# Kernel optimization log

Hardware: AMD Instinct MI355X
Metric: run time of the kernel (lower is better)

Reference implementation:

```python
import jax, jax.numpy as jnp
import numpy as np

B, A, S, IN, H, OUT, T = 32768, 10, 50, 6, 64, 2, 60


def _p(key, shape, scale=0.1):
    return (jax.random.normal(key, shape) * scale).astype(jnp.float32)


def setup_inputs() -> dict:
    key = jax.random.key(0)
    ks = jax.random.split(key, 20)
    inp = {
        'history': jax.random.normal(ks[0], (B, A, S, IN), dtype=jnp.float32),
        # encoder layer 0 (IN->H) and layer 1 (H->H); PyTorch gate order i,f,g,o
        'enc_Wih0': _p(ks[1], (4 * H, IN)), 'enc_Whh0': _p(ks[2], (4 * H, H)),
        'enc_bih0': _p(ks[3], (4 * H,)),    'enc_bhh0': _p(ks[4], (4 * H,)),
        'enc_Wih1': _p(ks[5], (4 * H, H)),  'enc_Whh1': _p(ks[6], (4 * H, H)),
        'enc_bih1': _p(ks[7], (4 * H,)),    'enc_bhh1': _p(ks[8], (4 * H,)),
        # decoder layer 0 (OUT->H) and layer 1 (H->H)
        'dec_Wih0': _p(ks[9], (4 * H, OUT)), 'dec_Whh0': _p(ks[10], (4 * H, H)),
        'dec_bih0': _p(ks[11], (4 * H,)),    'dec_bhh0': _p(ks[12], (4 * H,)),
        'dec_Wih1': _p(ks[13], (4 * H, H)),  'dec_Whh1': _p(ks[14], (4 * H, H)),
        'dec_bih1': _p(ks[15], (4 * H,)),    'dec_bhh1': _p(ks[16], (4 * H,)),
        'lin_W': _p(ks[17], (OUT, H)), 'lin_b': _p(ks[18], (OUT,)),
        'start_token': _p(ks[19], (1, 1, OUT)),
    }
    return inp


def _cell(x, h, c, Wih, Whh, bih, bhh):
    g = x @ Wih.T + h @ Whh.T + (bih + bhh)
    i, f, gg, o = jnp.split(g, 4, axis=-1)
    c2 = jax.nn.sigmoid(f) * c + jax.nn.sigmoid(i) * jnp.tanh(gg)
    h2 = jax.nn.sigmoid(o) * jnp.tanh(c2)
    return h2, c2


def reference(history, enc_Wih0, enc_Whh0, enc_bih0, enc_bhh0,
              enc_Wih1, enc_Whh1, enc_bih1, enc_bhh1,
              dec_Wih0, dec_Whh0, dec_bih0, dec_bhh0,
              dec_Wih1, dec_Whh1, dec_bih1, dec_bhh1,
              lin_W, lin_b, start_token):
    ego = history[:, 0]                     # [B, S, IN]
    b = ego.shape[0]
    z = jnp.zeros((b, H), dtype=ego.dtype)

    def enc_step(carry, xt):
        h0, c0, h1, c1 = carry
        h0, c0 = _cell(xt, h0, c0, enc_Wih0, enc_Whh0, enc_bih0, enc_bhh0)
        h1, c1 = _cell(h0, h1, c1, enc_Wih1, enc_Whh1, enc_bih1, enc_bhh1)
        return (h0, c0, h1, c1), None

    (h0, c0, h1, c1), _ = jax.lax.scan(enc_step, (z, z, z, z),
                                       jnp.swapaxes(ego, 0, 1))  # time-major [S,B,IN]

    start = jnp.broadcast_to(start_token[0], (b, start_token.shape[2]))  # [B, OUT]

    def dec_step(carry, _):
        h0, c0, h1, c1, inp = carry
        h0, c0 = _cell(inp, h0, c0, dec_Wih0, dec_Whh0, dec_bih0, dec_bhh0)
        h1, c1 = _cell(h0, h1, c1, dec_Wih1, dec_Whh1, dec_bih1, dec_bhh1)
        out = h1 @ lin_W.T + lin_b           # [B, OUT]
        return (h0, c0, h1, c1, out), out

    _, preds = jax.lax.scan(dec_step, (h0, c0, h1, c1, start), None, length=T)
    return jnp.swapaxes(preds, 0, 1)         # [B, T, OUT]
```

## Files before the change

kernel.cpp:

```cpp
#include <hip/hip_runtime.h>
#include <stdint.h>

typedef float f32x4 __attribute__((ext_vector_type(4)));
typedef __bf16 bf16x8 __attribute__((ext_vector_type(8)));

#define SEQ 50
#define TDEC 60
#define XCH 10

static __device__ __forceinline__ float ex2(float x) { return __builtin_amdgcn_exp2f(x); }
static __device__ __forceinline__ float frcp_(float x) { return __builtin_amdgcn_rcpf(x); }
static __device__ __forceinline__ __bf16 bfc(float x) { return (__bf16)x; }

__global__ __launch_bounds__(256, 2) void lstm_s2s(
    const float* __restrict__ hist,
    const float* __restrict__ eWih0, const float* __restrict__ eWhh0,
    const float* __restrict__ ebih0, const float* __restrict__ ebhh0,
    const float* __restrict__ eWih1, const float* __restrict__ eWhh1,
    const float* __restrict__ ebih1, const float* __restrict__ ebhh1,
    const float* __restrict__ dWih0, const float* __restrict__ dWhh0,
    const float* __restrict__ dbih0, const float* __restrict__ dbhh0,
    const float* __restrict__ dWih1, const float* __restrict__ dWhh1,
    const float* __restrict__ dbih1, const float* __restrict__ dbhh1,
    const float* __restrict__ linW, const float* __restrict__ linb,
    const float* __restrict__ stok,
    float* __restrict__ out)
{
  __shared__ __bf16 xch[XCH * 64 * 8];
  __shared__ __bf16 hb0[2][4096];
  __shared__ __bf16 hb1[2][4096];
  __shared__ __bf16 obuf[64 * 8];
  __shared__ __bf16 wx0s[4 * 4 * 64 * 8];
  __shared__ __bf16 wlc[128];

  const int tid = threadIdx.x;
  const int lane = tid & 63;
  const int w = tid >> 6;
  const int c = lane & 15;
  const int q = lane >> 4;
  const long rowbase = (long)blockIdx.x * 64;
  const float* eg = hist + rowbase * 3000;

  bf16x8 zfrag;
#pragma unroll
  for (int j = 0; j < 8; ++j) zfrag[j] = (__bf16)0.0f;
  f32x4 zero4;
  zero4[0] = 0.f; zero4[1] = 0.f; zero4[2] = 0.f; zero4[3] = 0.f;

  const float GS[4] = {-1.442695041f, -1.442695041f, 2.885390082f, -1.442695041f};

  bf16x8 whL0[4][2], wxL1[4][2], whL1[4][2];
  float bs1[4];

  auto loadFull = [&](const float* W, bf16x8 (*dst)[2]) {
#pragma unroll
    for (int g = 0; g < 4; ++g)
#pragma unroll
      for (int kc = 0; kc < 2; ++kc) {
        const float* p = W + ((g * 4 + w) * 16 + c) * 64 + kc * 32 + q * 8;
        f32x4 a = *(const f32x4*)p;
        f32x4 b = *(const f32x4*)(p + 4);
        bf16x8 f;
        f[0] = bfc(GS[g] * a[0]); f[1] = bfc(GS[g] * a[1]);
        f[2] = bfc(GS[g] * a[2]); f[3] = bfc(GS[g] * a[3]);
        f[4] = bfc(GS[g] * b[0]); f[5] = bfc(GS[g] * b[1]);
        f[6] = bfc(GS[g] * b[2]); f[7] = bfc(GS[g] * b[3]);
        dst[g][kc] = f;
      }
  };
  auto loadBias = [&](const float* bi, const float* bh, float* bs) {
#pragma unroll
    for (int g = 0; g < 4; ++g) {
      int n = g * 64 + w * 16 + c;
      bs[g] = GS[g] * (bi[n] + bh[n]);
    }
  };
  auto stageWx0 = [&](const float* W, int Kin, const float* bi, const float* bh) {
    for (int s = tid; s < 1024; s += 256) {
      int w2 = s >> 8;
      int g = (s >> 6) & 3;
      int ln = s & 63;
      int cc = ln & 15, qq = ln >> 4;
      float gs = (g == 2) ? 2.885390082f : -1.442695041f;
      __bf16* dst = wx0s + s * 8;
      int row = (g * 4 + w2) * 16 + cc;
      if (qq == 0) {
        for (int j = 0; j < 8; ++j) {
          float v = 0.0f;
          if (j < Kin) v = W[row * Kin + j];
          else if (j == 6) v = bi[row] + bh[row];
          dst[j] = bfc(gs * v);
        }
      } else {
        for (int j = 0; j < 8; ++j) dst[j] = (__bf16)0.0f;
      }
    }
  };
  auto stageX = [&](int t0) {
    for (int i = tid; i < XCH * 64 * 8; i += 256) {
      int k = i & 7;
      int row = (i >> 3) & 63;
      int tl = i >> 9;
      float v;
      if (k < 6) v = eg[row * 3000 + (t0 + tl) * 6 + k];
      else v = (k == 6) ? 1.0f : 0.0f;
      xch[i] = bfc(v);
    }
  };

  const int u = w * 16 + c;
  const int wconst = (u >> 5) * 2048 + ((u >> 3) & 3) * 128 + q * 32 + (u & 7);

  float cs0[16], cs1[16];
#pragma unroll
  for (int i = 0; i < 16; ++i) { cs0[i] = 0.0f; cs1[i] = 0.0f; }

  auto epilogue = [&](f32x4 (*acc)[4], __bf16* hnxt, float* cs) {
#pragma unroll
    for (int mt = 0; mt < 4; ++mt)
#pragma unroll
      for (int r = 0; r < 4; ++r) {
        float eI = ex2(acc[0][mt][r]);
        float eF = ex2(acc[1][mt][r]);
        float eG = ex2(acc[2][mt][r]);
        float eO = ex2(acc[3][mt][r]);
        float cc = cs[mt * 4 + r];
        float c2 = frcp_(1.0f + eF) * cc +
                   (eG - 1.0f) * frcp_((1.0f + eI) * (eG + 1.0f));
        float eC = ex2(2.885390082f * c2);
        float h2 = (eC - 1.0f) * frcp_((1.0f + eO) * (eC + 1.0f));
        cs[mt * 4 + r] = c2;
        hnxt[wconst + mt * 512 + r * 8] = bfc(h2);
      }
    __syncthreads();
  };

  auto cellP = [&](const __bf16* xsrc, const __bf16* hcur, __bf16* hnxt, float* cs) {
    bf16x8 wxf[4];
#pragma unroll
    for (int g = 0; g < 4; ++g)
      wxf[g] = *(const bf16x8*)(wx0s + (w * 256 + g * 64 + lane) * 8);
    f32x4 acc[4][4];
#pragma unroll
    for (int mt = 0; mt < 4; ++mt) {
      bf16x8 xf = zfrag;
      if (q == 0) xf = *(const bf16x8*)(xsrc + (mt * 16 + c) * 8);
#pragma unroll
      for (int g = 0; g < 4; ++g)
        acc[g][mt] = __builtin_amdgcn_mfma_f32_16x16x32_bf16(xf, wxf[g], zero4, 0, 0, 0),
        (void)0;
    }
#pragma unroll
    for (int kc = 0; kc < 2; ++kc)
#pragma unroll
      for (int mt = 0; mt < 4; ++mt) {
        bf16x8 hf = *(const bf16x8*)(hcur + (kc * 4 + mt) * 512 + lane * 8);
#pragma unroll
        for (int g = 0; g < 4; ++g)
          acc[g][mt] = __builtin_amdgcn_mfma_f32_16x16x32_bf16(hf, whL0[g][kc], acc[g][mt], 0, 0, 0);
      }
    epilogue(acc, hnxt, cs);
  };

  auto cellF = [&](const __bf16* xcur, const __bf16* hcur, __bf16* hnxt, float* cs) {
    f32x4 acc[4][4];
#pragma unroll
    for (int g = 0; g < 4; ++g) {
      float b = bs1[g];
#pragma unroll
      for (int mt = 0; mt < 4; ++mt) {
        acc[g][mt][0] = b; acc[g][mt][1] = b; acc[g][mt][2] = b; acc[g][mt][3] = b;
      }
    }
#pragma unroll
    for (int kc = 0; kc < 2; ++kc)
#pragma unroll
      for (int mt = 0; mt < 4; ++mt) {
        bf16x8 xf = *(const bf16x8*)(xcur + (kc * 4 + mt) * 512 + lane * 8);
#pragma unroll
        for (int g = 0; g < 4; ++g)
          acc[g][mt] = __builtin_amdgcn_mfma_f32_16x16x32_bf16(xf, wxL1[g][kc], acc[g][mt], 0, 0, 0);
      }
#pragma unroll
    for (int kc = 0; kc < 2; ++kc)
#pragma unroll
      for (int mt = 0; mt < 4; ++mt) {
        bf16x8 hf = *(const bf16x8*)(hcur + (kc * 4 + mt) * 512 + lane * 8);
#pragma unroll
        for (int g = 0; g < 4; ++g)
          acc[g][mt] = __builtin_amdgcn_mfma_f32_16x16x32_bf16(hf, whL1[g][kc], acc[g][mt], 0, 0, 0);
      }
    epilogue(acc, hnxt, cs);
  };

  for (int i = tid; i < 2048; i += 256) {
    ((unsigned int*)hb0[0])[i] = 0u;
    ((unsigned int*)hb1[0])[i] = 0u;
  }

  stageWx0(eWih0, 6, ebih0, ebhh0);
  loadFull(eWhh0, whL0);
  loadFull(eWih1, wxL1);
  loadFull(eWhh1, whL1);
  loadBias(ebih1, ebhh1, bs1);

  int pc = 0;
#pragma unroll 1
  for (int t = 0; t < SEQ; ++t) {
    if ((t % XCH) == 0) {
      stageX(t);
      __syncthreads();
    }
    cellP(xch + (t % XCH) * 512, hb0[pc], hb0[pc ^ 1], cs0);
    cellF(hb0[pc ^ 1], hb1[pc], hb1[pc ^ 1], cs1);
    pc ^= 1;
  }

  stageWx0(dWih0, 2, dbih0, dbhh0);
  loadFull(dWhh0, whL0);
  loadFull(dWih1, wxL1);
  loadFull(dWhh1, whL1);
  loadBias(dbih1, dbhh1, bs1);

  for (int i = tid; i < 128; i += 256) {
    int kc = i >> 6, cc = (i >> 5) & 1, kk = i & 31;
    wlc[(kc * 2 + cc) * 32 + kk] = bfc(linW[cc * 64 + kc * 32 + kk]);
  }
  const float lb = (c < 2) ? linb[c] : 0.0f;
  {
    float s0 = stok[0], s1 = stok[1];
    for (int i = tid; i < 64; i += 256) {
      obuf[i * 8 + 0] = bfc(s0);
      obuf[i * 8 + 1] = bfc(s1);
      obuf[i * 8 + 2] = (__bf16)0.0f;
      obuf[i * 8 + 3] = (__bf16)0.0f;
      obuf[i * 8 + 4] = (__bf16)0.0f;
      obuf[i * 8 + 5] = (__bf16)0.0f;
      obuf[i * 8 + 6] = (__bf16)1.0f;
      obuf[i * 8 + 7] = (__bf16)0.0f;
    }
  }
  __syncthreads();

#pragma unroll 1
  for (int t = 0; t < TDEC; ++t) {
    cellP(obuf, hb0[pc], hb0[pc ^ 1], cs0);
    cellF(hb0[pc ^ 1], hb1[pc], hb1[pc ^ 1], cs1);
    {
      f32x4 oa;
      oa[0] = lb; oa[1] = lb; oa[2] = lb; oa[3] = lb;
#pragma unroll
      for (int kc = 0; kc < 2; ++kc) {
        bf16x8 hf = *(const bf16x8*)(hb1[pc ^ 1] + (kc * 4 + w) * 512 + lane * 8);
        bf16x8 wf = zfrag;
        if (c < 2) wf = *(const bf16x8*)(wlc + (kc * 2 + c) * 32 + q * 8);
        oa = __builtin_amdgcn_mfma_f32_16x16x32_bf16(hf, wf, oa, 0, 0, 0);
      }
      if (c < 2) {
#pragma unroll
        for (int r = 0; r < 4; ++r) {
          int row = w * 16 + q * 4 + r;
          float v = oa[r];
          out[(rowbase + row) * 120 + t * 2 + c] = v;
          obuf[row * 8 + c] = bfc(v);
        }
      }
    }
    __syncthreads();
    pc ^= 1;
  }
}

extern "C" void kernel_launch(void* const* d_in, const int* in_sizes, int n_in,
                              void* d_out, int out_size, void* d_ws, size_t ws_size,
                              hipStream_t stream) {
  (void)in_sizes; (void)n_in; (void)d_ws; (void)ws_size; (void)out_size;
  const float* p[20];
  for (int i = 0; i < 20; ++i) p[i] = (const float*)d_in[i];
  dim3 grid(512), block(256);
  hipLaunchKernelGGL(lstm_s2s, grid, block, 0, stream,
                     p[0], p[1], p[2], p[3], p[4], p[5], p[6], p[7], p[8], p[9],
                     p[10], p[11], p[12], p[13], p[14], p[15], p[16], p[17], p[18], p[19],
                     (float*)d_out);
}
```

Measured before the change: 1.165 ms.

## Shrink block batch to 16 rows with transposed MFMA and more blocks

Each block now handles 16 batch rows instead of 64, so the grid grows to 2048 blocks and launch bounds allow 3 blocks per CU. The MFMA operands are transposed so weights are the A operand and hidden state the B operand. The layer-1 bias is folded in through an extra MFMA against a ones fragment, and the whole 50-step input sequence is staged into LDS once. Per-thread accumulators and cell state shrink from 16 to 4 values, which cuts register pressure and raises occupancy. In exchange, each block does less MFMA work per sync, so per-step barrier and LDS latency weigh more, and weights are reloaded four times as often overall.

Result: faster. 1.045 ms (-10.3%).

```diff
diff --git a/kernel.cpp b/kernel.cpp
--- a/kernel.cpp
+++ b/kernel.cpp
@@ -3,16 +3,16 @@
 
 typedef float f32x4 __attribute__((ext_vector_type(4)));
 typedef __bf16 bf16x8 __attribute__((ext_vector_type(8)));
+typedef __bf16 bf16x4 __attribute__((ext_vector_type(4)));
 
 #define SEQ 50
 #define TDEC 60
-#define XCH 10
-
-static __device__ __forceinline__ float ex2(float x) { return __builtin_amdgcn_exp2f(x); }
-static __device__ __forceinline__ float frcp_(float x) { return __builtin_amdgcn_rcpf(x); }
-static __device__ __forceinline__ __bf16 bfc(float x) { return (__bf16)x; }
-
-__global__ __launch_bounds__(256, 2) void lstm_s2s(
+
+static __device__ __forceinline__ float ex2(float x){return __builtin_amdgcn_exp2f(x);}
+static __device__ __forceinline__ float frcp_(float x){return __builtin_amdgcn_rcpf(x);}
+static __device__ __forceinline__ __bf16 bfc(float x){return (__bf16)x;}
+
+__global__ __launch_bounds__(256,3) void lstm_s2s(
     const float* __restrict__ hist,
     const float* __restrict__ eWih0, const float* __restrict__ eWhh0,
     const float* __restrict__ ebih0, const float* __restrict__ ebhh0,
@@ -26,244 +26,234 @@
     const float* __restrict__ stok,
     float* __restrict__ out)
 {
-  __shared__ __bf16 xch[XCH * 64 * 8];
-  __shared__ __bf16 hb0[2][4096];
-  __shared__ __bf16 hb1[2][4096];
-  __shared__ __bf16 obuf[64 * 8];
-  __shared__ __bf16 wx0s[4 * 4 * 64 * 8];
-  __shared__ __bf16 wlc[128];
+  __shared__ __bf16 xch[SEQ*16*8];
+  __shared__ __bf16 hb0[2][1024];
+  __shared__ __bf16 hb1[2][1024];
+  __shared__ __bf16 wx0s[4*4*17*8];
+  __shared__ __bf16 bf1s[4*4*17*8];
+  __shared__ __bf16 wlc[2*3*4*8];
+  __shared__ __bf16 obuf[16*8];
 
   const int tid = threadIdx.x;
   const int lane = tid & 63;
   const int w = tid >> 6;
   const int c = lane & 15;
   const int q = lane >> 4;
-  const long rowbase = (long)blockIdx.x * 64;
+  const int rsel = (q == 0) ? c : 16;
+  const long rowbase = (long)blockIdx.x * 16;
   const float* eg = hist + rowbase * 3000;
 
-  bf16x8 zfrag;
-#pragma unroll
-  for (int j = 0; j < 8; ++j) zfrag[j] = (__bf16)0.0f;
-  f32x4 zero4;
-  zero4[0] = 0.f; zero4[1] = 0.f; zero4[2] = 0.f; zero4[3] = 0.f;
-
-  const float GS[4] = {-1.442695041f, -1.442695041f, 2.885390082f, -1.442695041f};
+  union { f32x4 f; bf16x8 h; } Z;
+  Z.f[0]=0.f; Z.f[1]=0.f; Z.f[2]=0.f; Z.f[3]=0.f;
+  const f32x4 zero4 = Z.f;
+  const bf16x8 zfrag = Z.h;
+  bf16x8 onef = zfrag;
+  if (q == 0) onef[0] = (__bf16)1.0f;
+
+  const float GS[4] = {-1.442695041f,-1.442695041f,2.885390082f,-1.442695041f};
+
+  for (int i = tid; i < 16*300; i += 256) {
+    int row = i / 300, o = i - row*300;
+    int t = o / 6, k = o - t*6;
+    xch[(t*16+row)*8 + k] = bfc(eg[row*3000 + o]);
+  }
+  for (int i = tid; i < 16*SEQ; i += 256) {
+    xch[i*8+6] = (__bf16)1.0f;
+    xch[i*8+7] = (__bf16)0.0f;
+  }
+  for (int i = tid; i < 512; i += 256) {
+    ((uint32_t*)hb0[0])[i] = 0u;
+    ((uint32_t*)hb1[0])[i] = 0u;
+  }
+
+  auto stageWx0 = [&](const float* W, int Kin, const float* bi, const float* bh) {
+    for (int i = tid; i < 272; i += 256) {
+      int w2 = i / 68, rem = i - w2*68;
+      int g = rem / 17, row = rem - g*17;
+      __bf16* dst = wx0s + i*8;
+      if (row < 16) {
+        int gate = (g*4 + w2)*16 + row;
+        float gs = (g==2) ? 2.885390082f : -1.442695041f;
+        for (int j = 0; j < 8; ++j) {
+          float v = 0.f;
+          if (j < Kin) v = W[gate*Kin + j];
+          else if (j == 6) v = bi[gate] + bh[gate];
+          dst[j] = bfc(gs*v);
+        }
+      } else {
+        for (int j = 0; j < 8; ++j) dst[j] = (__bf16)0.f;
+      }
+    }
+  };
+  auto stageBf1 = [&](const float* bi, const float* bh) {
+    for (int i = tid; i < 272; i += 256) {
+      int w2 = i / 68, rem = i - w2*68;
+      int g = rem / 17, row = rem - g*17;
+      __bf16* dst = bf1s + i*8;
+      float v = 0.f;
+      if (row < 16) {
+        int gate = (g*4 + w2)*16 + row;
+        float gs = (g==2) ? 2.885390082f : -1.442695041f;
+        v = gs*(bi[gate] + bh[gate]);
+      }
+      dst[0] = bfc(v);
+      for (int j = 1; j < 8; ++j) dst[j] = (__bf16)0.f;
+    }
+  };
 
   bf16x8 whL0[4][2], wxL1[4][2], whL1[4][2];
-  float bs1[4];
-
   auto loadFull = [&](const float* W, bf16x8 (*dst)[2]) {
 #pragma unroll
     for (int g = 0; g < 4; ++g)
 #pragma unroll
       for (int kc = 0; kc < 2; ++kc) {
-        const float* p = W + ((g * 4 + w) * 16 + c) * 64 + kc * 32 + q * 8;
+        const float* p = W + ((g*4 + w)*16 + c)*64 + kc*32 + q*8;
         f32x4 a = *(const f32x4*)p;
         f32x4 b = *(const f32x4*)(p + 4);
         bf16x8 f;
-        f[0] = bfc(GS[g] * a[0]); f[1] = bfc(GS[g] * a[1]);
-        f[2] = bfc(GS[g] * a[2]); f[3] = bfc(GS[g] * a[3]);
-        f[4] = bfc(GS[g] * b[0]); f[5] = bfc(GS[g] * b[1]);
-        f[6] = bfc(GS[g] * b[2]); f[7] = bfc(GS[g] * b[3]);
+        f[0]=bfc(GS[g]*a[0]); f[1]=bfc(GS[g]*a[1]);
+        f[2]=bfc(GS[g]*a[2]); f[3]=bfc(GS[g]*a[3]);
+        f[4]=bfc(GS[g]*b[0]); f[5]=bfc(GS[g]*b[1]);
+        f[6]=bfc(GS[g]*b[2]); f[7]=bfc(GS[g]*b[3]);
         dst[g][kc] = f;
       }
   };
-  auto loadBias = [&](const float* bi, const float* bh, float* bs) {
+
+  const int wconst = (w>>1)*512 + (((w&1)<<1) | (q>>1))*128 + c*8 + (q&1)*4;
+
+  float cs0[4], cs1[4];
+#pragma unroll
+  for (int i = 0; i < 4; ++i) { cs0[i] = 0.f; cs1[i] = 0.f; }
+
+  auto epilogue = [&](f32x4* a, float* cs, __bf16* hnxt) {
+    bf16x4 hv;
+#pragma unroll
+    for (int r = 0; r < 4; ++r) {
+      float eI = ex2(a[0][r]);
+      float eF = ex2(a[1][r]);
+      float eG = ex2(a[2][r]);
+      float eO = ex2(a[3][r]);
+      float P  = (1.f+eI)*(eG+1.f);
+      float tt = 1.f+eF;
+      float D  = frcp_(tt*P);
+      float c2 = (cs[r]*P + (eG-1.f)*tt)*D;
+      float eC = ex2(2.885390082f*c2);
+      float h2 = (eC-1.f)*frcp_((1.f+eO)*(eC+1.f));
+      cs[r] = c2;
+      hv[r] = bfc(h2);
+    }
+    *(bf16x4*)(hnxt + wconst) = hv;
+    __syncthreads();
+  };
+
+  auto cellP = [&](const __bf16* xsrc, const __bf16* hcur, __bf16* hnxt, float* cs) {
+    bf16x8 xf = zfrag;
+    if (q == 0) xf = *(const bf16x8*)(xsrc + c*8);
+    bf16x8 hf0 = *(const bf16x8*)(hcur + lane*8);
+    bf16x8 hf1 = *(const bf16x8*)(hcur + 512 + lane*8);
+    f32x4 a[4];
 #pragma unroll
     for (int g = 0; g < 4; ++g) {
-      int n = g * 64 + w * 16 + c;
-      bs[g] = GS[g] * (bi[n] + bh[n]);
-    }
-  };
-  auto stageWx0 = [&](const float* W, int Kin, const float* bi, const float* bh) {
-    for (int s = tid; s < 1024; s += 256) {
-      int w2 = s >> 8;
-      int g = (s >> 6) & 3;
-      int ln = s & 63;
-      int cc = ln & 15, qq = ln >> 4;
-      float gs = (g == 2) ? 2.885390082f : -1.442695041f;
-      __bf16* dst = wx0s + s * 8;
-      int row = (g * 4 + w2) * 16 + cc;
-      if (qq == 0) {
-        for (int j = 0; j < 8; ++j) {
-          float v = 0.0f;
-          if (j < Kin) v = W[row * Kin + j];
-          else if (j == 6) v = bi[row] + bh[row];
-          dst[j] = bfc(gs * v);
-        }
-      } else {
-        for (int j = 0; j < 8; ++j) dst[j] = (__bf16)0.0f;
-      }
-    }
-  };
-  auto stageX = [&](int t0) {
-    for (int i = tid; i < XCH * 64 * 8; i += 256) {
-      int k = i & 7;
-      int row = (i >> 3) & 63;
-      int tl = i >> 9;
-      float v;
-      if (k < 6) v = eg[row * 3000 + (t0 + tl) * 6 + k];
-      else v = (k == 6) ? 1.0f : 0.0f;
-      xch[i] = bfc(v);
-    }
-  };
-
-  const int u = w * 16 + c;
-  const int wconst = (u >> 5) * 2048 + ((u >> 3) & 3) * 128 + q * 32 + (u & 7);
-
-  float cs0[16], cs1[16];
-#pragma unroll
-  for (int i = 0; i < 16; ++i) { cs0[i] = 0.0f; cs1[i] = 0.0f; }
-
-  auto epilogue = [&](f32x4 (*acc)[4], __bf16* hnxt, float* cs) {
-#pragma unroll
-    for (int mt = 0; mt < 4; ++mt)
-#pragma unroll
-      for (int r = 0; r < 4; ++r) {
-        float eI = ex2(acc[0][mt][r]);
-        float eF = ex2(acc[1][mt][r]);
-        float eG = ex2(acc[2][mt][r]);
-        float eO = ex2(acc[3][mt][r]);
-        float cc = cs[mt * 4 + r];
-        float c2 = frcp_(1.0f + eF) * cc +
-                   (eG - 1.0f) * frcp_((1.0f + eI) * (eG + 1.0f));
-        float eC = ex2(2.885390082f * c2);
-        float h2 = (eC - 1.0f) * frcp_((1.0f + eO) * (eC + 1.0f));
-        cs[mt * 4 + r] = c2;
-        hnxt[wconst + mt * 512 + r * 8] = bfc(h2);
-      }
-    __syncthreads();
-  };
-
-  auto cellP = [&](const __bf16* xsrc, const __bf16* hcur, __bf16* hnxt, float* cs) {
-    bf16x8 wxf[4];
-#pragma unroll
-    for (int g = 0; g < 4; ++g)
-      wxf[g] = *(const bf16x8*)(wx0s + (w * 256 + g * 64 + lane) * 8);
-    f32x4 acc[4][4];
-#pragma unroll
-    for (int mt = 0; mt < 4; ++mt) {
-      bf16x8 xf = zfrag;
-      if (q == 0) xf = *(const bf16x8*)(xsrc + (mt * 16 + c) * 8);
-#pragma unroll
-      for (int g = 0; g < 4; ++g)
-        acc[g][mt] = __builtin_amdgcn_mfma_f32_16x16x32_bf16(xf, wxf[g], zero4, 0, 0, 0),
-        (void)0;
-    }
-#pragma unroll
-    for (int kc = 0; kc < 2; ++kc)
-#pragma unroll
-      for (int mt = 0; mt < 4; ++mt) {
-        bf16x8 hf = *(const bf16x8*)(hcur + (kc * 4 + mt) * 512 + lane * 8);
-#pragma unroll
-        for (int g = 0; g < 4; ++g)
-          acc[g][mt] = __builtin_amdgcn_mfma_f32_16x16x32_bf16(hf, whL0[g][kc], acc[g][mt], 0, 0, 0);
-      }
-    epilogue(acc, hnxt, cs);
+      bf16x8 wxf = *(const bf16x8*)(wx0s + ((w*4+g)*17 + rsel)*8);
+      a[g] = __builtin_amdgcn_mfma_f32_16x16x32_bf16(wxf, xf, zero4, 0,0,0);
+    }
+#pragma unroll
+    for (int g = 0; g < 4; ++g)
+      a[g] = __builtin_amdgcn_mfma_f32_16x16x32_bf16(whL0[g][0], hf0, a[g], 0,0,0);
+#pragma unroll
+    for (int g = 0; g < 4; ++g)
+      a[g] = __builtin_amdgcn_mfma_f32_16x16x32_bf16(whL0[g][1], hf1, a[g], 0,0,0);
+    epilogue(a, cs, hnxt);
   };
 
   auto cellF = [&](const __bf16* xcur, const __bf16* hcur, __bf16* hnxt, float* cs) {
-    f32x4 acc[4][4];
+    bf16x8 xf0 = *(const bf16x8*)(xcur + lane*8);
+    bf16x8 xf1 = *(const bf16x8*)(xcur + 512 + lane*8);
+    bf16x8 hf0 = *(const bf16x8*)(hcur + lane*8);
+    bf16x8 hf1 = *(const bf16x8*)(hcur + 512 + lane*8);
+    f32x4 a[4];
 #pragma unroll
     for (int g = 0; g < 4; ++g) {
-      float b = bs1[g];
-#pragma unroll
-      for (int mt = 0; mt < 4; ++mt) {
-        acc[g][mt][0] = b; acc[g][mt][1] = b; acc[g][mt][2] = b; acc[g][mt][3] = b;
-      }
-    }
-#pragma unroll
-    for (int kc = 0; kc < 2; ++kc)
-#pragma unroll
-      for (int mt = 0; mt < 4; ++mt) {
-        bf16x8 xf = *(const bf16x8*)(xcur + (kc * 4 + mt) * 512 + lane * 8);
-#pragma unroll
-        for (int g = 0; g < 4; ++g)
-          acc[g][mt] = __builtin_amdgcn_mfma_f32_16x16x32_bf16(xf, wxL1[g][kc], acc[g][mt], 0, 0, 0);
-      }
-#pragma unroll
-    for (int kc = 0; kc < 2; ++kc)
-#pragma unroll
-      for (int mt = 0; mt < 4; ++mt) {
-        bf16x8 hf = *(const bf16x8*)(hcur + (kc * 4 + mt) * 512 + lane * 8);
-#pragma unroll
-        for (int g = 0; g < 4; ++g)
-          acc[g][mt] = __builtin_amdgcn_mfma_f32_16x16x32_bf16(hf, whL1[g][kc], acc[g][mt], 0, 0, 0);
-      }
-    epilogue(acc, hnxt, cs);
-  };
-
-  for (int i = tid; i < 2048; i += 256) {
-    ((unsigned int*)hb0[0])[i] = 0u;
-    ((unsigned int*)hb1[0])[i] = 0u;
-  }
+      bf16x8 bfr = *(const bf16x8*)(bf1s + ((w*4+g)*17 + rsel)*8);
+      a[g] = __builtin_amdgcn_mfma_f32_16x16x32_bf16(bfr, onef, zero4, 0,0,0);
+    }
+#pragma unroll
+    for (int g = 0; g < 4; ++g)
+      a[g] = __builtin_amdgcn_mfma_f32_16x16x32_bf16(wxL1[g][0], xf0, a[g], 0,0,0);
+#pragma unroll
+    for (int g = 0; g < 4; ++g)
+      a[g] = __builtin_amdgcn_mfma_f32_16x16x32_bf16(wxL1[g][1], xf1, a[g], 0,0,0);
+#pragma unroll
+    for (int g = 0; g < 4; ++g)
+      a[g] = __builtin_amdgcn_mfma_f32_16x16x32_bf16(whL1[g][0], hf0, a[g], 0,0,0);
+#pragma unroll
+    for (int g = 0; g < 4; ++g)
+      a[g] = __builtin_amdgcn_mfma_f32_16x16x32_bf16(whL1[g][1], hf1, a[g], 0,0,0);
+    epilogue(a, cs, hnxt);
+  };
 
   stageWx0(eWih0, 6, ebih0, ebhh0);
+  stageBf1(ebih1, ebhh1);
   loadFull(eWhh0, whL0);
   loadFull(eWih1, wxL1);
   loadFull(eWhh1, whL1);
-  loadBias(ebih1, ebhh1, bs1);
+  __syncthreads();
 
   int pc = 0;
 #pragma unroll 1
   for (int t = 0; t < SEQ; ++t) {
-    if ((t % XCH) == 0) {
-      stageX(t);
-      __syncthreads();
-    }
-    cellP(xch + (t % XCH) * 512, hb0[pc], hb0[pc ^ 1], cs0);
-    cellF(hb0[pc ^ 1], hb1[pc], hb1[pc ^ 1], cs1);
+    cellP(xch + t*128, hb0[pc], hb0[pc^1], cs0);
+    cellF(hb0[pc^1], hb1[pc], hb1[pc^1], cs1);
     pc ^= 1;
   }
 
   stageWx0(dWih0, 2, dbih0, dbhh0);
+  stageBf1(dbih1, dbhh1);
   loadFull(dWhh0, whL0);
   loadFull(dWih1, wxL1);
   loadFull(dWhh1, whL1);
-  loadBias(dbih1, dbhh1, bs1);
-
-  for (int i = tid; i < 128; i += 256) {
-    int kc = i >> 6, cc = (i >> 5) & 1, kk = i & 31;
-    wlc[(kc * 2 + cc) * 32 + kk] = bfc(linW[cc * 64 + kc * 32 + kk]);
-  }
-  const float lb = (c < 2) ? linb[c] : 0.0f;
+  for (int i = tid; i < 24; i += 256) {
+    int kc = i / 12, rem = i - kc*12;
+    int row = rem / 4, q2 = rem - row*4;
+    __bf16* dst = wlc + i*8;
+    for (int j = 0; j < 8; ++j)
+      dst[j] = (row < 2) ? bfc(linW[row*64 + kc*32 + q2*8 + j]) : (__bf16)0.f;
+  }
   {
     float s0 = stok[0], s1 = stok[1];
-    for (int i = tid; i < 64; i += 256) {
-      obuf[i * 8 + 0] = bfc(s0);
-      obuf[i * 8 + 1] = bfc(s1);
-      obuf[i * 8 + 2] = (__bf16)0.0f;
-      obuf[i * 8 + 3] = (__bf16)0.0f;
-      obuf[i * 8 + 4] = (__bf16)0.0f;
-      obuf[i * 8 + 5] = (__bf16)0.0f;
-      obuf[i * 8 + 6] = (__bf16)1.0f;
-      obuf[i * 8 + 7] = (__bf16)0.0f;
-    }
-  }
+    for (int i = tid; i < 16; i += 256) {
+      obuf[i*8+0] = bfc(s0);
+      obuf[i*8+1] = bfc(s1);
+      obuf[i*8+2] = (__bf16)0.f;
+      obuf[i*8+3] = (__bf16)0.f;
+      obuf[i*8+4] = (__bf16)0.f;
+      obuf[i*8+5] = (__bf16)0.f;
+      obuf[i*8+6] = (__bf16)1.0f;
+      obuf[i*8+7] = (__bf16)0.f;
+    }
+  }
+  const float lb0 = linb[0], lb1 = linb[1];
   __syncthreads();
 
 #pragma unroll 1
   for (int t = 0; t < TDEC; ++t) {
-    cellP(obuf, hb0[pc], hb0[pc ^ 1], cs0);
-    cellF(hb0[pc ^ 1], hb1[pc], hb1[pc ^ 1], cs1);
-    {
-      f32x4 oa;
-      oa[0] = lb; oa[1] = lb; oa[2] = lb; oa[3] = lb;
-#pragma unroll
-      for (int kc = 0; kc < 2; ++kc) {
-        bf16x8 hf = *(const bf16x8*)(hb1[pc ^ 1] + (kc * 4 + w) * 512 + lane * 8);
-        bf16x8 wf = zfrag;
-        if (c < 2) wf = *(const bf16x8*)(wlc + (kc * 2 + c) * 32 + q * 8);
-        oa = __builtin_amdgcn_mfma_f32_16x16x32_bf16(hf, wf, oa, 0, 0, 0);
-      }
-      if (c < 2) {
-#pragma unroll
-        for (int r = 0; r < 4; ++r) {
-          int row = w * 16 + q * 4 + r;
-          float v = oa[r];
-          out[(rowbase + row) * 120 + t * 2 + c] = v;
-          obuf[row * 8 + c] = bfc(v);
-        }
+    cellP(obuf, hb0[pc], hb0[pc^1], cs0);
+    cellF(hb0[pc^1], hb1[pc], hb1[pc^1], cs1);
+    if (w == 0) {
+      const __bf16* h1 = hb1[pc^1];
+      bf16x8 xf0 = *(const bf16x8*)(h1 + lane*8);
+      bf16x8 xf1 = *(const bf16x8*)(h1 + 512 + lane*8);
+      int hr = (c < 2) ? c : 2;
+      bf16x8 wl0 = *(const bf16x8*)(wlc + hr*32 + q*8);
+      bf16x8 wl1 = *(const bf16x8*)(wlc + 96 + hr*32 + q*8);
+      f32x4 oa = __builtin_amdgcn_mfma_f32_16x16x32_bf16(wl0, xf0, zero4, 0,0,0);
+      oa = __builtin_amdgcn_mfma_f32_16x16x32_bf16(wl1, xf1, oa, 0,0,0);
+      if (q == 0) {
+        float v0 = oa[0] + lb0, v1 = oa[1] + lb1;
+        float2 vv; vv.x = v0; vv.y = v1;
+        *(float2*)(out + (rowbase + c)*120 + t*2) = vv;
+        obuf[c*8+0] = bfc(v0);
+        obuf[c*8+1] = bfc(v1);
       }
     }
     __syncthreads();
@@ -277,7 +267,7 @@
   (void)in_sizes; (void)n_in; (void)d_ws; (void)ws_size; (void)out_size;
   const float* p[20];
   for (int i = 0; i < 20; ++i) p[i] = (const float*)d_in[i];
-  dim3 grid(512), block(256);
+  dim3 grid(2048), block(256);
   hipLaunchKernelGGL(lstm_s2s, grid, block, 0, stream,
                      p[0], p[1], p[2], p[3], p[4], p[5], p[6], p[7], p[8], p[9],
                      p[10], p[11], p[12], p[13], p[14], p[15], p[16], p[17], p[18], p[19],
```
